# Kernel tuning notes

Measured on AMD Instinct MI355X. Metric: run time of the kernel, lower is better.

Reference implementation:

```python
import jax, jax.numpy as jnp
import numpy as np

N = 100000
E = 1600000
IN_DIM = 128
HID = 128
OUT = 8


def _linear_params(key, fan_in, fan_out, bias=True):
    k1, k2 = jax.random.split(key)
    bound = 1.0 / np.sqrt(fan_in)
    W = jax.random.uniform(k1, (fan_in, fan_out), jnp.float32, -bound, bound)
    if bias:
        b = jax.random.uniform(k2, (fan_out,), jnp.float32, -bound, bound)
        return W, b
    return W


def setup_inputs() -> dict:
    key = jax.random.key(0)
    ks = jax.random.split(key, 20)
    x = jax.random.normal(ks[0], (N, IN_DIM), jnp.float32)
    edge_index = jax.random.randint(ks[1], (2, E), 0, N, jnp.int64)
    y = jax.random.randint(ks[2], (N,), 0, 2, jnp.int64)
    pmp_mask = jax.random.randint(ks[3], (N,), 0, 2, jnp.int64).astype(jnp.bool_)
    # layer 1 params
    W_fr1 = _linear_params(ks[4], IN_DIM, HID, bias=False)
    W_be1 = _linear_params(ks[5], IN_DIM, HID, bias=False)
    alpha_w1, alpha_b1 = _linear_params(ks[6], IN_DIM, 1)
    Wself_w1, Wself_b1 = _linear_params(ks[7], IN_DIM, HID)
    # layer 2 params
    W_fr2 = _linear_params(ks[8], HID, HID, bias=False)
    W_be2 = _linear_params(ks[9], HID, HID, bias=False)
    alpha_w2, alpha_b2 = _linear_params(ks[10], HID, 1)
    Wself_w2, Wself_b2 = _linear_params(ks[11], HID, HID)
    # classifier
    cls_w, cls_b = _linear_params(ks[12], HID, OUT)
    return dict(x=x, edge_index=edge_index, y=y, pmp_mask=pmp_mask,
                W_fr1=W_fr1, W_be1=W_be1, alpha_w1=alpha_w1, alpha_b1=alpha_b1,
                Wself_w1=Wself_w1, Wself_b1=Wself_b1,
                W_fr2=W_fr2, W_be2=W_be2, alpha_w2=alpha_w2, alpha_b2=alpha_b2,
                Wself_w2=Wself_w2, Wself_b2=Wself_b2,
                cls_w=cls_w, cls_b=cls_b)


def _pmp_layer(x, src, dst, node_type, W_fr, W_be, alpha_w, alpha_b, Wself_w, Wself_b):
    # alpha_mlp: Linear(in,1) -> sigmoid, per node
    alpha = jax.nn.sigmoid(x @ alpha_w + alpha_b)          # [N,1]
    xj = x[src]                                            # gather source feats [E,d]
    msg_fr = xj @ W_fr                                     # [E,h]
    msg_be = xj @ W_be                                     # [E,h]
    a = alpha[dst]                                         # gather target alpha [E,1]
    ntj = node_type[src][:, None]                          # [E,1]
    msg_un = a * msg_fr + (1.0 - a) * msg_be
    msg = jnp.where(ntj == 1, msg_fr, jnp.where(ntj == 0, msg_be, msg_un))
    aggr = jax.ops.segment_sum(msg, dst, num_segments=N)   # scatter-add into targets
    return aggr + x @ Wself_w + Wself_b


def reference(x, edge_index, y, pmp_mask,
              W_fr1, W_be1, alpha_w1, alpha_b1, Wself_w1, Wself_b1,
              W_fr2, W_be2, alpha_w2, alpha_b2, Wself_w2, Wself_b2,
              cls_w, cls_b):
    src, dst = edge_index[0], edge_index[1]  # PyG: row=source j, col=target i
    node_type = jnp.where(pmp_mask, y, jnp.full_like(y, 2))  # [N], in {0,1,2}
    h = _pmp_layer(x, src, dst, node_type, W_fr1, W_be1, alpha_w1, alpha_b1, Wself_w1, Wself_b1)
    h = jax.nn.relu(h)
    # dropout inactive (inference)
    h = _pmp_layer(h, src, dst, node_type, W_fr2, W_be2, alpha_w2, alpha_b2, Wself_w2, Wself_b2)
    h = jax.nn.relu(h)
    return h @ cls_w + cls_b
```

## Files before the change

kernel.cpp:

```cpp
#include <hip/hip_runtime.h>
#include <hip/hip_bf16.h>
#include <cmath>

#define DEV static __device__ __forceinline__

constexpr int NN = 100000;
constexpr int NN_PAD = 100352;
constexpr int NE = 1600000;
constexpr int D  = 128;
constexpr int KTOT = 384;
constexpr int SCHUNK = 1024;
constexpr int NBS = (NN + SCHUNK - 1) / SCHUNK;

typedef __attribute__((ext_vector_type(8))) short short8;
typedef __attribute__((ext_vector_type(4))) float f32x4;
typedef __attribute__((ext_vector_type(2))) float f32x2;
typedef __attribute__((ext_vector_type(16))) float f32x16;

DEV float bf2f(unsigned short u) {
    unsigned int t = ((unsigned int)u) << 16;
    return __builtin_bit_cast(float, t);
}
DEV unsigned short f2bf(float f) {
    unsigned int u = __builtin_bit_cast(unsigned int, f);
    u += 0x7fffu + ((u >> 16) & 1u);
    return (unsigned short)(u >> 16);
}
DEV unsigned int packbf(float a, float b) {
    return (unsigned int)f2bf(a) | ((unsigned int)f2bf(b) << 16);
}
DEV f32x2 pk_fma(f32x2 a, f32x2 b, f32x2 c) {
    f32x2 d;
    asm("v_pk_fma_f32 %0, %1, %2, %3" : "=v"(d) : "v"(a), "v"(b), "v"(c));
    return d;
}

__global__ void k_detect(const unsigned int* __restrict__ ew,
                         const unsigned int* __restrict__ yw,
                         const unsigned int* __restrict__ mw,
                         int* __restrict__ flags) {
    int lane = threadIdx.x & 63;
    int c_e = __popcll(__ballot(ew[2 * lane + 1] != 0u));
    int c_y = __popcll(__ballot(yw[2 * lane + 1] != 0u));
    int c_mb = __popcll(__ballot(mw[lane] > 1u));
    int c_mz = __popcll(__ballot(mw[2 * lane + 1] != 0u));
    if (lane == 0) {
        flags[1] = (c_e < 8) ? 1 : 0;
        flags[2] = (c_y < 8) ? 1 : 0;
        flags[3] = c_mb > 8 ? 2 : (c_mz < 8 ? 1 : 0);
    }
}

__global__ void k_prep(const int* __restrict__ flg, const void* __restrict__ y,
                       const void* __restrict__ mask, int* __restrict__ nt) {
    int i = blockIdx.x * blockDim.x + threadIdx.x;
    if (i >= NN) return;
    int yv = flg[2] ? (int)((const long long*)y)[i] : ((const int*)y)[i];
    int mm = flg[3] == 2 ? (int)((const unsigned char*)mask)[i]
           : flg[3] == 1 ? (int)((const long long*)mask)[i]
           : ((const int*)mask)[i];
    nt[i] = mm ? yv : 2;
}

__global__ void k_conv_e(const int* __restrict__ flg, const void* __restrict__ ei,
                         const int* __restrict__ nt,
                         int* __restrict__ SP, int* __restrict__ DST,
                         int* __restrict__ deg, int* __restrict__ rnk) {
    int e = blockIdx.x * blockDim.x + threadIdx.x;
    if (e >= NE) return;
    int s, d;
    if (flg[1]) {
        const long long* p = (const long long*)ei;
        s = (int)p[e]; d = (int)p[NE + e];
    } else {
        const int* p = (const int*)ei;
        s = p[e]; d = p[NE + e];
    }
    SP[e] = (s << 2) | nt[s];
    DST[e] = d;
    rnk[e] = atomicAdd(&deg[d], 1);
}

__global__ void k_convx(const float* __restrict__ x,
                        unsigned short* __restrict__ Ahi, unsigned short* __restrict__ XLO) {
    long t = blockIdx.x * (long)blockDim.x + threadIdx.x;
    long g = t * 4;
    if (g >= (long)NN * D) return;
    int n = (int)(g >> 7);
    int k = (int)(g & 127);
    float4 v = *(const float4*)(x + g);
    float vv[4] = {v.x, v.y, v.z, v.w};
    ushort4 hi, lo;
    unsigned short* hp = (unsigned short*)&hi;
    unsigned short* lp = (unsigned short*)&lo;
#pragma unroll
    for (int j = 0; j < 4; j++) {
        unsigned short h = f2bf(vv[j]);
        hp[j] = h;
        lp[j] = f2bf(vv[j] - bf2f(h));
    }
    *(ushort4*)(Ahi + (size_t)n * KTOT + k) = hi;
    *(ushort4*)(XLO + (size_t)n * D + k) = lo;
}

__global__ void k_wprep(const float* __restrict__ Wsf, const float* __restrict__ Wfr,
                        const float* __restrict__ Wbe,
                        unsigned short* __restrict__ WpHi, unsigned short* __restrict__ WpLo) {
    int t = blockIdx.x * blockDim.x + threadIdx.x;
    if (t >= KTOT * D) return;
    int k = t >> 7;
    int c = t & 127;
    float w = k < 128 ? Wsf[k * 128 + c]
            : k < 256 ? Wfr[(k - 128) * 128 + c]
            : Wbe[(k - 256) * 128 + c];
    unsigned short hi = f2bf(w);
    unsigned short lo = f2bf(w - bf2f(hi));
    int ks = k >> 4, kin = k & 15;
    int grp = kin >> 3, j = kin & 7;
    int ct = c >> 5, cl = c & 31;
    size_t idx = (((size_t)ks * 4 + ct) * 64 + ((grp << 5) | cl)) * 8 + j;
    WpHi[idx] = hi;
    WpLo[idx] = lo;
}

__global__ void k_scan_a(const int* __restrict__ deg, int* __restrict__ bsum) {
    __shared__ int sh[256];
    int b = blockIdx.x, t = threadIdx.x;
    int base = b * SCHUNK + t * 4;
    int s = 0;
#pragma unroll
    for (int j = 0; j < 4; j++) { int i = base + j; if (i < NN) s += deg[i]; }
    sh[t] = s; __syncthreads();
    for (int d = 128; d > 0; d >>= 1) {
        if (t < d) sh[t] += sh[t + d];
        __syncthreads();
    }
    if (t == 0) bsum[b] = sh[0];
}

__global__ void k_scan_b(const int* __restrict__ bsum, int* __restrict__ bpre,
                         int* __restrict__ offs) {
    __shared__ int sh[128];
    int t = threadIdx.x;
    int v = (t < NBS) ? bsum[t] : 0;
    int incl = v; sh[t] = incl; __syncthreads();
    for (int d = 1; d < 128; d <<= 1) {
        int add = (t >= d) ? sh[t - d] : 0;
        __syncthreads();
        incl += add; sh[t] = incl;
        __syncthreads();
    }
    if (t < NBS) bpre[t] = incl - v;
    if (t == 0) offs[NN] = NE;
}

__global__ void k_scan_c(const int* __restrict__ deg, const int* __restrict__ bpre,
                         int* __restrict__ offs) {
    __shared__ int sh[256];
    int b = blockIdx.x, t = threadIdx.x;
    int base = b * SCHUNK + t * 4;
    int v[4];
#pragma unroll
    for (int j = 0; j < 4; j++) { int i = base + j; v[j] = (i < NN) ? deg[i] : 0; }
    int tsum = v[0] + v[1] + v[2] + v[3];
    int incl = tsum; sh[t] = incl; __syncthreads();
    for (int d = 1; d < 256; d <<= 1) {
        int add = (t >= d) ? sh[t - d] : 0;
        __syncthreads();
        incl += add; sh[t] = incl;
        __syncthreads();
    }
    int ex = (incl - tsum) + bpre[b];
#pragma unroll
    for (int j = 0; j < 4; j++) {
        int i = base + j;
        if (i < NN) { offs[i] = ex; ex += v[j]; }
    }
}

__global__ void k_place(const int* __restrict__ SP, const int* __restrict__ DST,
                        const int* __restrict__ RNK, const int* __restrict__ offs,
                        int* __restrict__ ssrc) {
    for (int e = blockIdx.x * blockDim.x + threadIdx.x; e < NE; e += gridDim.x * blockDim.x) {
        int d = DST[e];
        int slot = offs[d] + RNK[e];
        __builtin_nontemporal_store(SP[e], &ssrc[slot]);
    }
}

__global__ void __launch_bounds__(256)
k_aggr(unsigned short* __restrict__ Ahi, const unsigned short* __restrict__ XLO,
       const int* __restrict__ sp, const int* __restrict__ offs,
       const float* __restrict__ aw, const float* __restrict__ ab) {
    int lane = threadIdx.x & 63;
    int d = blockIdx.x * (blockDim.x >> 6) + (threadIdx.x >> 6);
    if (d >= NN) return;
    int eg = lane >> 4;
    int dg = lane & 15;
    int k0 = dg * 8;

    int ak = lane * 2;
    unsigned int whi = *(const unsigned int*)(Ahi + d * KTOT + ak);
    unsigned int wlo = *(const unsigned int*)(XLO + d * D + ak);
    float xa = bf2f((unsigned short)(whi & 0xffffu)) + bf2f((unsigned short)(wlo & 0xffffu));
    float xb = bf2f((unsigned short)(whi >> 16)) + bf2f((unsigned short)(wlo >> 16));
    float dot = xa * aw[ak] + xb * aw[ak + 1];
#pragma unroll
    for (int m = 32; m > 0; m >>= 1) dot += __shfl_xor(dot, m, 64);
    float a = 1.0f / (1.0f + expf(-(dot + ab[0])));

    f32x2 u2[4], t2[4];
#pragma unroll
    for (int q = 0; q < 4; q++) { u2[q] = (f32x2){0.f, 0.f}; t2[q] = (f32x2){0.f, 0.f}; }

    int e0 = offs[d];
    int n = offs[d + 1] - e0;
    const int* spp = sp + e0;
    for (int base = 0; base < n; base += 16) {
        int ii[4], pk[4];
        float cu[4], ct[4];
        uint4 w[4];
#pragma unroll
        for (int s4 = 0; s4 < 4; s4++) {
            ii[s4] = base + 4 * s4 + eg;
            pk[s4] = spp[ii[s4] < n ? ii[s4] : 0];
        }
#pragma unroll
        for (int s4 = 0; s4 < 4; s4++) {
            int b = pk[s4] & 3;
            int src = pk[s4] >> 2;
            bool vv = ii[s4] < n;
            cu[s4] = vv ? (b == 1 ? 1.f : (b == 2 ? a : 0.f)) : 0.f;
            ct[s4] = vv ? 1.f : 0.f;
            w[s4] = *(const uint4*)(Ahi + (src * KTOT + k0));
        }
#pragma unroll
        for (int s4 = 0; s4 < 4; s4++) {
            f32x2 cu2 = (f32x2){cu[s4], cu[s4]};
            f32x2 ct2 = (f32x2){ct[s4], ct[s4]};
            const unsigned int* wp = (const unsigned int*)&w[s4];
#pragma unroll
            for (int q = 0; q < 4; q++) {
                f32x2 xv = (f32x2){bf2f((unsigned short)(wp[q] & 0xffffu)),
                                   bf2f((unsigned short)(wp[q] >> 16))};
                u2[q] = pk_fma(xv, cu2, u2[q]);
                t2[q] = pk_fma(xv, ct2, t2[q]);
            }
        }
    }

#pragma unroll
    for (int q = 0; q < 4; q++) {
        u2[q].x += __shfl_xor(u2[q].x, 16, 64);
        u2[q].x += __shfl_xor(u2[q].x, 32, 64);
        u2[q].y += __shfl_xor(u2[q].y, 16, 64);
        u2[q].y += __shfl_xor(u2[q].y, 32, 64);
        t2[q].x += __shfl_xor(t2[q].x, 16, 64);
        t2[q].x += __shfl_xor(t2[q].x, 32, 64);
        t2[q].y += __shfl_xor(t2[q].y, 16, 64);
        t2[q].y += __shfl_xor(t2[q].y, 32, 64);
    }
    if (eg == 0) {
        unsigned int up[4], vp[4];
#pragma unroll
        for (int q = 0; q < 4; q++) {
            up[q] = packbf(u2[q].x, u2[q].y);
            vp[q] = packbf(t2[q].x - u2[q].x, t2[q].y - u2[q].y);
        }
        *(uint4*)(Ahi + (d * KTOT + 128 + k0)) = *(uint4*)up;
        *(uint4*)(Ahi + (d * KTOT + 256 + k0)) = *(uint4*)vp;
    }
}

template<int WRITE_LO>
__global__ void __launch_bounds__(256)
k_mfma(unsigned short* __restrict__ Ahi, unsigned short* __restrict__ XLO,
       const unsigned short* __restrict__ WpHi, const unsigned short* __restrict__ WpLo,
       const float* __restrict__ bias) {
    int lane = threadIdx.x & 63;
    int wave = threadIdx.x >> 6;
    int r0 = blockIdx.x * 128 + wave * 32;

    int mrow = lane & 31, kg = lane >> 5;
    const unsigned short* aHiB = Ahi + (size_t)(r0 + mrow) * KTOT + kg * 8;
    const unsigned short* aLoB = XLO + (size_t)(r0 + mrow) * D + kg * 8;

    f32x16 acc[4];
#pragma unroll
    for (int i = 0; i < 4; i++) acc[i] = (f32x16)(0.f);

    short8 bh[4], bl[4];
#pragma unroll
    for (int ct = 0; ct < 4; ct++) {
        int wb = (ct * 64 + lane) * 8;
        bh[ct] = *(const short8*)(WpHi + wb);
        bl[ct] = *(const short8*)(WpLo + wb);
    }

#pragma unroll
    for (int ks = 0; ks < 24; ks++) {
        short8 nbh[4], nbl[4];
        if (ks < 23) {
#pragma unroll
            for (int ct = 0; ct < 4; ct++) {
                int wb = (((ks + 1) * 4 + ct) * 64 + lane) * 8;
                nbh[ct] = *(const short8*)(WpHi + wb);
                nbl[ct] = *(const short8*)(WpLo + wb);
            }
        }
        short8 ah = *(const short8*)(aHiB + ks * 16);
        short8 al;
        if (ks < 8) al = *(const short8*)(aLoB + ks * 16);
#pragma unroll
        for (int ct = 0; ct < 4; ct++) {
            acc[ct] = __builtin_amdgcn_mfma_f32_32x32x16_bf16(ah, bh[ct], acc[ct], 0, 0, 0);
            acc[ct] = __builtin_amdgcn_mfma_f32_32x32x16_bf16(ah, bl[ct], acc[ct], 0, 0, 0);
            if (ks < 8)
                acc[ct] = __builtin_amdgcn_mfma_f32_32x32x16_bf16(al, bh[ct], acc[ct], 0, 0, 0);
        }
        if (ks < 23) {
#pragma unroll
            for (int ct = 0; ct < 4; ct++) { bh[ct] = nbh[ct]; bl[ct] = nbl[ct]; }
        }
    }

    int ccol = lane & 31;
    int rbase = 4 * (lane >> 5);
#pragma unroll
    for (int ct = 0; ct < 4; ct++) {
        float bb = bias[ct * 32 + ccol];
#pragma unroll
        for (int reg = 0; reg < 16; reg++) {
            int row = r0 + rbase + (reg & 3) + 8 * (reg >> 2);
            float v = fmaxf(acc[ct][reg] + bb, 0.f);
            unsigned short h = f2bf(v);
            Ahi[(size_t)row * KTOT + ct * 32 + ccol] = h;
            if (WRITE_LO) {
                unsigned short l = f2bf(v - bf2f(h));
                XLO[(size_t)row * D + ct * 32 + ccol] = l;
            }
        }
    }
}

__global__ void __launch_bounds__(256)
k_cls(const unsigned short* __restrict__ Ahi,
      const float* __restrict__ W, const float* __restrict__ b, float* __restrict__ out) {
    int lane = threadIdx.x & 63;
    int wid = blockIdx.x * (blockDim.x >> 6) + (threadIdx.x >> 6);
    if (wid >= NN) return;
    int cc = lane & 7;
    int kg = lane >> 3;
    const unsigned short* hH = Ahi + (size_t)wid * KTOT + kg * 16;
    float s = 0.f;
#pragma unroll
    for (int j = 0; j < 16; j += 2) {
        unsigned int ph = *(const unsigned int*)(hH + j);
        float h0 = bf2f((unsigned short)(ph & 0xffffu));
        float h1 = bf2f((unsigned short)(ph >> 16));
        s += h0 * W[(kg * 16 + j) * 8 + cc];
        s += h1 * W[(kg * 16 + j + 1) * 8 + cc];
    }
    s += __shfl_xor(s, 8, 64);
    s += __shfl_xor(s, 16, 64);
    s += __shfl_xor(s, 32, 64);
    if (lane < 8) out[(size_t)wid * 8 + cc] = s + b[cc];
}

extern "C" void kernel_launch(void* const* d_in, const int* in_sizes, int n_in,
                              void* d_out, int out_size, void* d_ws, size_t ws_size,
                              hipStream_t stream) {
    const float* x   = (const float*)d_in[0];
    const void* ei   = d_in[1];
    const void* y    = d_in[2];
    const void* mask = d_in[3];

    char* ws = (char*)d_ws;
    size_t cur_off = 0;
    auto alloc = [&](size_t bytes) {
        size_t o = cur_off;
        cur_off = (cur_off + bytes + 255) & ~(size_t)255;
        return o;
    };

    size_t oAhi = alloc((size_t)NN_PAD * KTOT * 2);
    size_t oXLO = alloc((size_t)NN_PAD * D * 2);
    size_t oW1h = alloc(KTOT * D * 2);
    size_t oW1l = alloc(KTOT * D * 2);
    size_t oW2h = alloc(KTOT * D * 2);
    size_t oW2l = alloc(KTOT * D * 2);
    size_t oNT   = alloc(NN * 4);
    size_t oDEG  = alloc(NN * 4);
    size_t oOFFS = alloc((NN + 1) * 4);
    size_t oBSUM = alloc(NBS * 4);
    size_t oBPRE = alloc(NBS * 4);
    size_t oSP   = alloc((size_t)NE * 4);
    size_t oDST  = alloc((size_t)NE * 4);
    size_t oRNK  = alloc((size_t)NE * 4);
    size_t oSSRC = alloc((size_t)NE * 4);
    size_t oFLG  = alloc(256);

    unsigned short* Ahi = (unsigned short*)(ws + oAhi);
    unsigned short* XLO = (unsigned short*)(ws + oXLO);
    unsigned short* W1h = (unsigned short*)(ws + oW1h);
    unsigned short* W1l = (unsigned short*)(ws + oW1l);
    unsigned short* W2h = (unsigned short*)(ws + oW2h);
    unsigned short* W2l = (unsigned short*)(ws + oW2l);
    int* NT   = (int*)(ws + oNT);
    int* DEG  = (int*)(ws + oDEG);
    int* OFFS = (int*)(ws + oOFFS);
    int* BSUM = (int*)(ws + oBSUM);
    int* BPRE = (int*)(ws + oBPRE);
    int* SP   = (int*)(ws + oSP);
    int* DST  = (int*)(ws + oDST);
    int* RNK  = (int*)(ws + oRNK);
    int* SSRC = (int*)(ws + oSSRC);
    int* FLG  = (int*)(ws + oFLG);

    hipMemsetAsync(DEG, 0, NN * sizeof(int), stream);

    k_detect<<<1, 64, 0, stream>>>((const unsigned int*)ei, (const unsigned int*)y,
                                   (const unsigned int*)mask, FLG);
    k_prep<<<(NN + 255) / 256, 256, 0, stream>>>(FLG, y, mask, NT);
    k_conv_e<<<(NE + 255) / 256, 256, 0, stream>>>(FLG, ei, NT, SP, DST, DEG, RNK);
    k_convx<<<NN * D / 4 / 256, 256, 0, stream>>>(x, Ahi, XLO);
    k_wprep<<<(KTOT * D + 255) / 256, 256, 0, stream>>>(
        (const float*)d_in[8], (const float*)d_in[4], (const float*)d_in[5], W1h, W1l);
    k_wprep<<<(KTOT * D + 255) / 256, 256, 0, stream>>>(
        (const float*)d_in[14], (const float*)d_in[10], (const float*)d_in[11], W2h, W2l);

    k_scan_a<<<NBS, 256, 0, stream>>>(DEG, BSUM);
    k_scan_b<<<1, 128, 0, stream>>>(BSUM, BPRE, OFFS);
    k_scan_c<<<NBS, 256, 0, stream>>>(DEG, BPRE, OFFS);
    k_place<<<2048, 256, 0, stream>>>(SP, DST, RNK, OFFS, SSRC);

    k_aggr<<<NN / 4, 256, 0, stream>>>(Ahi, XLO, SSRC, OFFS,
        (const float*)d_in[6], (const float*)d_in[7]);
    k_mfma<1><<<NN_PAD / 128, 256, 0, stream>>>(Ahi, XLO, W1h, W1l, (const float*)d_in[9]);
    k_aggr<<<NN / 4, 256, 0, stream>>>(Ahi, XLO, SSRC, OFFS,
        (const float*)d_in[12], (const float*)d_in[13]);
    k_mfma<0><<<NN_PAD / 128, 256, 0, stream>>>(Ahi, XLO, W2h, W2l, (const float*)d_in[15]);

    k_cls<<<NN / 4, 256, 0, stream>>>(Ahi, (const float*)d_in[16],
                                      (const float*)d_in[17], (float*)d_out);
}
```

Baseline: 432.5 us.

## Fuse classifier into second MFMA epilogue and node-type prep into edge conversion

The classifier matmul is folded into the epilogue of the second-layer MFMA kernel, so each wave reduces ReLU outputs against the 128x8 classifier weights with cross-lane shuffles and writes the final output directly. This removes the bf16 write of layer-2 hidden state and the separate k_cls launch that re-read it. It also computes the node type inline in k_conv_e from y and mask gathered at the source index, dropping the k_prep kernel and NT buffer. The costs are many shuffles in the epilogue, per-edge random reads of y and mask in place of one int array, and the classifier now reading the fp32 activation rather than its bf16 rounding.

New measurement: 424.1 us. No clear change (-1.9%).

```diff
diff --git a/kernel.cpp b/kernel.cpp
--- a/kernel.cpp
+++ b/kernel.cpp
@@ -51,19 +51,8 @@
     }
 }
 
-__global__ void k_prep(const int* __restrict__ flg, const void* __restrict__ y,
-                       const void* __restrict__ mask, int* __restrict__ nt) {
-    int i = blockIdx.x * blockDim.x + threadIdx.x;
-    if (i >= NN) return;
-    int yv = flg[2] ? (int)((const long long*)y)[i] : ((const int*)y)[i];
-    int mm = flg[3] == 2 ? (int)((const unsigned char*)mask)[i]
-           : flg[3] == 1 ? (int)((const long long*)mask)[i]
-           : ((const int*)mask)[i];
-    nt[i] = mm ? yv : 2;
-}
-
 __global__ void k_conv_e(const int* __restrict__ flg, const void* __restrict__ ei,
-                         const int* __restrict__ nt,
+                         const void* __restrict__ y, const void* __restrict__ mask,
                          int* __restrict__ SP, int* __restrict__ DST,
                          int* __restrict__ deg, int* __restrict__ rnk) {
     int e = blockIdx.x * blockDim.x + threadIdx.x;
@@ -76,7 +65,12 @@
         const int* p = (const int*)ei;
         s = p[e]; d = p[NE + e];
     }
-    SP[e] = (s << 2) | nt[s];
+    int yv = flg[2] ? (int)((const long long*)y)[s] : ((const int*)y)[s];
+    int mm = flg[3] == 2 ? (int)((const unsigned char*)mask)[s]
+           : flg[3] == 1 ? (int)((const long long*)mask)[s]
+           : ((const int*)mask)[s];
+    int nt = mm ? yv : 2;
+    SP[e] = (s << 2) | nt;
     DST[e] = d;
     rnk[e] = atomicAdd(&deg[d], 1);
 }
@@ -272,11 +266,13 @@
     }
 }
 
-template<int WRITE_LO>
+template<int MODE>
 __global__ void __launch_bounds__(256)
 k_mfma(unsigned short* __restrict__ Ahi, unsigned short* __restrict__ XLO,
        const unsigned short* __restrict__ WpHi, const unsigned short* __restrict__ WpLo,
-       const float* __restrict__ bias) {
+       const float* __restrict__ bias,
+       const float* __restrict__ cw, const float* __restrict__ cb,
+       float* __restrict__ out) {
     int lane = threadIdx.x & 63;
     int wave = threadIdx.x >> 6;
     int r0 = blockIdx.x * 128 + wave * 32;
@@ -326,45 +322,49 @@
 
     int ccol = lane & 31;
     int rbase = 4 * (lane >> 5);
-#pragma unroll
-    for (int ct = 0; ct < 4; ct++) {
-        float bb = bias[ct * 32 + ccol];
+    if (MODE == 0) {
+#pragma unroll
+        for (int ct = 0; ct < 4; ct++) {
+            float bb = bias[ct * 32 + ccol];
+#pragma unroll
+            for (int reg = 0; reg < 16; reg++) {
+                int row = r0 + rbase + (reg & 3) + 8 * (reg >> 2);
+                float v = fmaxf(acc[ct][reg] + bb, 0.f);
+                unsigned short h = f2bf(v);
+                Ahi[(size_t)row * KTOT + ct * 32 + ccol] = h;
+                unsigned short l = f2bf(v - bf2f(h));
+                XLO[(size_t)row * D + ct * 32 + ccol] = l;
+            }
+        }
+    } else {
+        float bb[4];
+#pragma unroll
+        for (int ct = 0; ct < 4; ct++) bb[ct] = bias[ct * 32 + ccol];
+        int l32 = lane & 31;
 #pragma unroll
         for (int reg = 0; reg < 16; reg++) {
             int row = r0 + rbase + (reg & 3) + 8 * (reg >> 2);
-            float v = fmaxf(acc[ct][reg] + bb, 0.f);
-            unsigned short h = f2bf(v);
-            Ahi[(size_t)row * KTOT + ct * 32 + ccol] = h;
-            if (WRITE_LO) {
-                unsigned short l = f2bf(v - bf2f(h));
-                XLO[(size_t)row * D + ct * 32 + ccol] = l;
-            }
-        }
-    }
-}
-
-__global__ void __launch_bounds__(256)
-k_cls(const unsigned short* __restrict__ Ahi,
-      const float* __restrict__ W, const float* __restrict__ b, float* __restrict__ out) {
-    int lane = threadIdx.x & 63;
-    int wid = blockIdx.x * (blockDim.x >> 6) + (threadIdx.x >> 6);
-    if (wid >= NN) return;
-    int cc = lane & 7;
-    int kg = lane >> 3;
-    const unsigned short* hH = Ahi + (size_t)wid * KTOT + kg * 16;
-    float s = 0.f;
-#pragma unroll
-    for (int j = 0; j < 16; j += 2) {
-        unsigned int ph = *(const unsigned int*)(hH + j);
-        float h0 = bf2f((unsigned short)(ph & 0xffffu));
-        float h1 = bf2f((unsigned short)(ph >> 16));
-        s += h0 * W[(kg * 16 + j) * 8 + cc];
-        s += h1 * W[(kg * 16 + j + 1) * 8 + cc];
-    }
-    s += __shfl_xor(s, 8, 64);
-    s += __shfl_xor(s, 16, 64);
-    s += __shfl_xor(s, 32, 64);
-    if (lane < 8) out[(size_t)wid * 8 + cc] = s + b[cc];
+            float p[8];
+#pragma unroll
+            for (int cc = 0; cc < 8; cc++) p[cc] = 0.f;
+#pragma unroll
+            for (int ct = 0; ct < 4; ct++) {
+                float v = fmaxf(acc[ct][reg] + bb[ct], 0.f);
+                const float* wrow = cw + (ct * 32 + l32) * 8;
+#pragma unroll
+                for (int cc = 0; cc < 8; cc++) p[cc] += v * wrow[cc];
+            }
+#pragma unroll
+            for (int m = 1; m < 32; m <<= 1) {
+#pragma unroll
+                for (int cc = 0; cc < 8; cc++) p[cc] += __shfl_xor(p[cc], m, 64);
+            }
+            if (l32 == 0 && row < NN) {
+#pragma unroll
+                for (int cc = 0; cc < 8; cc++) out[(size_t)row * 8 + cc] = p[cc] + cb[cc];
+            }
+        }
+    }
 }
 
 extern "C" void kernel_launch(void* const* d_in, const int* in_sizes, int n_in,
@@ -389,7 +389,6 @@
     size_t oW1l = alloc(KTOT * D * 2);
     size_t oW2h = alloc(KTOT * D * 2);
     size_t oW2l = alloc(KTOT * D * 2);
-    size_t oNT   = alloc(NN * 4);
     size_t oDEG  = alloc(NN * 4);
     size_t oOFFS = alloc((NN + 1) * 4);
     size_t oBSUM = alloc(NBS * 4);
@@ -406,7 +405,6 @@
     unsigned short* W1l = (unsigned short*)(ws + oW1l);
     unsigned short* W2h = (unsigned short*)(ws + oW2h);
     unsigned short* W2l = (unsigned short*)(ws + oW2l);
-    int* NT   = (int*)(ws + oNT);
     int* DEG  = (int*)(ws + oDEG);
     int* OFFS = (int*)(ws + oOFFS);
     int* BSUM = (int*)(ws + oBSUM);
@@ -421,8 +419,7 @@
 
     k_detect<<<1, 64, 0, stream>>>((const unsigned int*)ei, (const unsigned int*)y,
                                    (const unsigned int*)mask, FLG);
-    k_prep<<<(NN + 255) / 256, 256, 0, stream>>>(FLG, y, mask, NT);
-    k_conv_e<<<(NE + 255) / 256, 256, 0, stream>>>(FLG, ei, NT, SP, DST, DEG, RNK);
+    k_conv_e<<<(NE + 255) / 256, 256, 0, stream>>>(FLG, ei, y, mask, SP, DST, DEG, RNK);
     k_convx<<<NN * D / 4 / 256, 256, 0, stream>>>(x, Ahi, XLO);
     k_wprep<<<(KTOT * D + 255) / 256, 256, 0, stream>>>(
         (const float*)d_in[8], (const float*)d_in[4], (const float*)d_in[5], W1h, W1l);
@@ -436,11 +433,11 @@
 
     k_aggr<<<NN / 4, 256, 0, stream>>>(Ahi, XLO, SSRC, OFFS,
         (const float*)d_in[6], (const float*)d_in[7]);
-    k_mfma<1><<<NN_PAD / 128, 256, 0, stream>>>(Ahi, XLO, W1h, W1l, (const float*)d_in[9]);
+    k_mfma<0><<<NN_PAD / 128, 256, 0, stream>>>(Ahi, XLO, W1h, W1l,
+        (const float*)d_in[9], nullptr, nullptr, nullptr);
     k_aggr<<<NN / 4, 256, 0, stream>>>(Ahi, XLO, SSRC, OFFS,
         (const float*)d_in[12], (const float*)d_in[13]);
-    k_mfma<0><<<NN_PAD / 128, 256, 0, stream>>>(Ahi, XLO, W2h, W2l, (const float*)d_in[15]);
-
-    k_cls<<<NN / 4, 256, 0, stream>>>(Ahi, (const float*)d_in[16],
-                                      (const float*)d_in[17], (float*)d_out);
-}
+    k_mfma<1><<<NN_PAD / 128, 256, 0, stream>>>(Ahi, XLO, W2h, W2l,
+        (const float*)d_in[15], (const float*)d_in[16], (const float*)d_in[17],
+        (float*)d_out);
+}
```
